# Performance work log

Measured on AMD Instinct MI355X. Metric: run time of the kernel, lower is better.

The kernel has to match this reference:

```python
import jax, jax.numpy as jnp
import numpy as np

N_NODES = 100000
N_EDGES = 1600000
N_GRAPHS = 1024
HID = 128
NODE_DIM = 7
EDGE_DIM = 3
LAYERS = 4
LN_EPS = 1e-5


def setup_inputs() -> dict:
    key = jax.random.key(0)
    ks = jax.random.split(key, 24)
    s = lambda i, shape, scale=0.05: (jax.random.normal(ks[i], shape, dtype=jnp.float32) * scale)
    x = jax.random.normal(ks[0], (N_NODES, NODE_DIM), dtype=jnp.float32)
    edge_index = jax.random.randint(ks[1], (2, N_EDGES), 0, N_NODES, dtype=jnp.int32)
    edge_attr = jax.random.normal(ks[2], (N_EDGES, EDGE_DIM), dtype=jnp.float32)
    batch = jnp.sort(jax.random.randint(ks[3], (N_NODES,), 0, N_GRAPHS, dtype=jnp.int32))
    return {
        'x': x, 'edge_index': edge_index, 'edge_attr': edge_attr, 'batch': batch,
        'inW': s(4, (NODE_DIM, HID)), 'inb': s(5, (HID,)),
        'edgeW': s(6, (LAYERS, EDGE_DIM, HID)), 'edgeb': s(7, (LAYERS, HID)),
        'w1': s(8, (LAYERS, HID, HID)), 'b1': s(9, (LAYERS, HID)),
        'w2': s(10, (LAYERS, HID, HID)), 'b2': s(11, (LAYERS, HID)),
        'gamma': jnp.ones((LAYERS, HID), dtype=jnp.float32),
        'beta': jnp.zeros((LAYERS, HID), dtype=jnp.float32),
        'fcW1': s(12, (HID, HID)), 'fcb1': s(13, (HID,)),
        'fcW2': s(14, (HID, HID // 2)), 'fcb2': s(15, (HID // 2,)),
        'fcW3': s(16, (HID // 2, 1)), 'fcb3': s(17, (1,)),
    }


def _layernorm(x, gamma, beta):
    mu = jnp.mean(x, axis=-1, keepdims=True)
    var = jnp.mean(jnp.square(x - mu), axis=-1, keepdims=True)
    return (x - mu) * jax.lax.rsqrt(var + LN_EPS) * gamma + beta


def reference(x, edge_index, edge_attr, batch, inW, inb, edgeW, edgeb,
              w1, b1, w2, b2, gamma, beta, fcW1, fcb1, fcW2, fcb2, fcW3, fcb3):
    src, dst = edge_index[0], edge_index[1]
    h = x @ inW + inb  # [N, HID]
    for l in range(LAYERS):
        e = edge_attr @ edgeW[l] + edgeb[l]              # [E, HID]
        msg = jax.nn.relu(h[src] + e)                    # gather + relu
        agg = jax.ops.segment_sum(msg, dst, num_segments=N_NODES)  # scatter-add
        g = agg + h                                      # (1+eps)*x_r with eps=0
        g = jax.nn.relu(g @ w1[l] + b1[l]) @ w2[l] + b2[l]  # GINE MLP
        h = _layernorm(h + jax.nn.relu(g), gamma[l], beta[l])  # residual + LN
    # global mean pool over graphs
    sums = jax.ops.segment_sum(h, batch, num_segments=N_GRAPHS)
    cnt = jax.ops.segment_sum(jnp.ones((h.shape[0],), h.dtype), batch, num_segments=N_GRAPHS)
    pooled = sums / jnp.maximum(cnt, 1.0)[:, None]
    # head (dropout is identity in eval)
    o = jax.nn.relu(pooled @ fcW1 + fcb1)
    o = jax.nn.relu(o @ fcW2 + fcb2)
    return o @ fcW3 + fcb3  # [N_GRAPHS, 1]
```

## Files before the change

kernel.cpp:

```cpp
#include <hip/hip_runtime.h>

#define N_NODES 100000
#define N_EDGES 1600000
#define N_GRAPHS 1024
#define HID 128
#define LAYERS 4
#define LN_EPS 1e-5f
#define GTS 136
#define NB_PROJ 50000
#define NB_WCONV 512
#define NBUCK 1563
#define BCAP 2048
#define NSTREAM 8
#define CURPAD 32
#define EPB 4096
#define NB_BS 391


typedef __attribute__((ext_vector_type(8))) short bf16x8;
typedef __attribute__((ext_vector_type(4))) float f32x4;

__device__ __forceinline__ unsigned short f2bf(float x) {
    unsigned v = __float_as_uint(x);
    return (unsigned short)((v + 0x7fffu + ((v >> 16) & 1u)) >> 16);
}
__device__ __forceinline__ float bfval(unsigned short u) {
    return __uint_as_float((unsigned)u << 16);
}

__global__ __launch_bounds__(256) void k_prep(
    const float* __restrict__ x, const float* __restrict__ inW,
    const float* __restrict__ inb, float* __restrict__ h,
    unsigned short* __restrict__ hb,
    const float* __restrict__ w1, const float* __restrict__ w2,
    unsigned short* __restrict__ wf_hi, unsigned short* __restrict__ wf_lo) {
    if (blockIdx.x < NB_PROJ) {
        int idx = blockIdx.x * 256 + threadIdx.x;
        int n = idx >> 7, c = idx & 127;
        const float* xr = x + n * 7;
        float s = inb[c];
#pragma unroll
        for (int k = 0; k < 7; ++k) s += xr[k] * inW[k * HID + c];
        h[idx] = s;
        hb[idx] = f2bf(s);
    } else {
        int idx = (blockIdx.x - NB_PROJ) * 256 + threadIdx.x;
        int wid = idx >> 14;
        int layer = wid >> 1, which = wid & 1;
        int within = idx & 16383;
        int nt = within >> 11;
        int ks = (within >> 9) & 3;
        int ln = (within >> 3) & 63;
        int j = within & 7;
        const float* W = (which ? w2 : w1) + layer * HID * HID;
        int k = ks * 32 + (ln >> 4) * 8 + j;
        int n = nt * 16 + (ln & 15);
        float v = W[k * HID + n];
        unsigned short hi = f2bf(v);
        wf_hi[idx] = hi;
        wf_lo[idx] = f2bf(v - bfval(hi));
    }
}

__global__ __launch_bounds__(256) void k_hist(
    const int* __restrict__ ei, int* __restrict__ cnt2) {
    __shared__ int hcnt[NBUCK];
    const int t = threadIdx.x;
    for (int i = t; i < NBUCK; i += 256) hcnt[i] = 0;
    __syncthreads();
    const int e0 = blockIdx.x * EPB;
    const int eend = (e0 + EPB < N_EDGES) ? e0 + EPB : N_EDGES;
#pragma unroll
    for (int k = 0; k < 16; ++k) {
        const int e = e0 + k * 256 + t;
        if (e < eend) atomicAdd(&hcnt[ei[N_EDGES + e] >> 6], 1);
    }
    __syncthreads();
    const int sgrp = blockIdx.x & 7;
    for (int i = t; i < NBUCK; i += 256) {
        const int c = hcnt[i];
        if (c) atomicAdd(&cnt2[((i << 3) + sgrp) << 5], c);
    }
}

__global__ __launch_bounds__(1024) void k_segscan(
    const int* __restrict__ cnt2, int* __restrict__ pcur,
    int* __restrict__ bucket_base, int* __restrict__ row_ptr) {
    __shared__ int lsum[1024];
    const int t = threadIdx.x;
    const int b0 = 2 * t, b1 = 2 * t + 1;
    int u0 = 0, u1 = 0;
    if (b0 < NBUCK) {
#pragma unroll
        for (int s = 0; s < NSTREAM; ++s) u0 += cnt2[((b0 << 3) + s) << 5];
    }
    if (b1 < NBUCK) {
#pragma unroll
        for (int s = 0; s < NSTREAM; ++s) u1 += cnt2[((b1 << 3) + s) << 5];
    }
    const int v = u0 + u1;
    lsum[t] = v;
    __syncthreads();
    for (int off = 1; off < 1024; off <<= 1) {
        const int u = (t >= off) ? lsum[t - off] : 0;
        __syncthreads();
        lsum[t] += u;
        __syncthreads();
    }
    const int excl = lsum[t] - v;
    if (b0 < NBUCK) {
        bucket_base[b0] = excl;
        int run = excl;
#pragma unroll
        for (int s = 0; s < NSTREAM; ++s) {
            const int c = ((b0 << 3) + s) << 5;
            pcur[c] = run;
            run += cnt2[c];
        }
    }
    if (b1 < NBUCK) {
        const int base1 = excl + u0;
        bucket_base[b1] = base1;
        int run = base1;
#pragma unroll
        for (int s = 0; s < NSTREAM; ++s) {
            const int c = ((b1 << 3) + s) << 5;
            pcur[c] = run;
            run += cnt2[c];
        }
    }
    if (t == 0) {
        bucket_base[NBUCK] = N_EDGES;
        row_ptr[N_NODES] = N_EDGES;
    }
}

__global__ __launch_bounds__(256) void k_binscat(
    const int* __restrict__ ei, const float* __restrict__ ea,
    int* __restrict__ pcur, int4* __restrict__ erec) {
    __shared__ int hcnt[NBUCK];
    const int t = threadIdx.x;
    for (int i = t; i < NBUCK; i += 256) hcnt[i] = 0;
    __syncthreads();
    const int e0 = blockIdx.x * EPB;
    const int eend = (e0 + EPB < N_EDGES) ? e0 + EPB : N_EDGES;
#pragma unroll
    for (int k = 0; k < 16; ++k) {
        const int e = e0 + k * 256 + t;
        if (e < eend) atomicAdd(&hcnt[ei[N_EDGES + e] >> 6], 1);
    }
    __syncthreads();
    const int sgrp = blockIdx.x & 7;
    for (int i = t; i < NBUCK; i += 256) {
        const int c = hcnt[i];
        hcnt[i] = c ? atomicAdd(&pcur[((i << 3) + sgrp) << 5], c) : 0;
    }
    __syncthreads();
#pragma unroll
    for (int k = 0; k < 16; ++k) {
        const int e = e0 + k * 256 + t;
        if (e < eend) {
            const int src = ei[e];
            const int dst = ei[N_EDGES + e];
            const float a0 = ea[e * 3 + 0];
            const float a1 = ea[e * 3 + 1];
            const float a2 = ea[e * 3 + 2];
            const int pos = atomicAdd(&hcnt[dst >> 6], 1);
            int4 r;
            r.x = src | ((dst & 63) << 20);
            r.y = __float_as_int(a0);
            r.z = __float_as_int(a1);
            r.w = __float_as_int(a2);
            erec[pos] = r;
        }
    }
}

__global__ __launch_bounds__(256) void k_bucketsort(
    const int4* __restrict__ erec, const int* __restrict__ bucket_base,
    int* __restrict__ row_ptr, int* __restrict__ esrc,
    float* __restrict__ eattr) {
    __shared__ int rhist[64];
    __shared__ int lcur[64];
    __shared__ int4 stage[BCAP];
    const int b = blockIdx.x;
    const int nb0 = b << 6;
    const int nrows = (nb0 + 64 <= N_NODES) ? 64 : (N_NODES - nb0);
    const int base = bucket_base[b];
    const int end = bucket_base[b + 1];
    const int cnt = end - base;
    const int t = threadIdx.x;
    if (t < 64) rhist[t] = 0;
    __syncthreads();
    for (int i = t; i < cnt; i += 256)
        atomicAdd(&rhist[(erec[base + i].x >> 20) & 63], 1);
    __syncthreads();
    if (t < 64) {
        const int v = rhist[t];
        int incl = v;
#pragma unroll
        for (int off = 1; off < 64; off <<= 1) {
            const int u = __shfl_up(incl, off);
            if (t >= off) incl += u;
        }
        const int excl = incl - v;
        lcur[t] = excl;
        if (t < nrows) row_ptr[nb0 + t] = base + excl;
    }
    __syncthreads();
    if (cnt <= BCAP) {
        for (int i = t; i < cnt; i += 256) {
            const int4 r = erec[base + i];
            stage[atomicAdd(&lcur[(r.x >> 20) & 63], 1)] = r;
        }
        __syncthreads();
        for (int i = t; i < cnt; i += 256)
            esrc[base + i] = stage[i].x & 0xFFFFF;
        float* ef = eattr + (size_t)base * 3;
        const float* sf = (const float*)stage;
        const int m = cnt * 3;
        for (int i = t; i < m; i += 256)
            ef[i] = sf[(i / 3) * 4 + 1 + (i % 3)];
    } else {
        for (int i = t; i < cnt; i += 256) {
            const int4 r = erec[base + i];
            const int pos = base + atomicAdd(&lcur[(r.x >> 20) & 63], 1);
            esrc[pos] = r.x & 0xFFFFF;
            eattr[(size_t)pos * 3 + 0] = __int_as_float(r.y);
            eattr[(size_t)pos * 3 + 1] = __int_as_float(r.z);
            eattr[(size_t)pos * 3 + 2] = __int_as_float(r.w);
        }
    }
}

#define FLUSHSTEP {                                                            \
    if (rcur == 0)      { a0x = ax; a0y = ay; rnext = rp2; }                   \
    else if (rcur == 1) { a1x = ax; a1y = ay; rnext = rp3; }                   \
    else                { a2x = ax; a2y = ay; rnext = 0x7fffffff; }            \
    ax = 0.f; ay = 0.f; ++rcur; }

#define EL(JJ)                                                                 \
    const int s##JJ = __builtin_amdgcn_readlane(cS, j + JJ);                   \
    const unsigned gq##JJ = *(const unsigned*)(hbin + (long)s##JJ * HID + c2);

#define EC(JJ) {                                                               \
    const int gi = t + j + (JJ);                                               \
    while (gi >= rnext) FLUSHSTEP                                              \
    const float ax_ = __uint_as_float(__builtin_amdgcn_readlane(__float_as_int(cA0), j + JJ)); \
    const float ay_ = __uint_as_float(__builtin_amdgcn_readlane(__float_as_int(cA1), j + JJ)); \
    const float az_ = __uint_as_float(__builtin_amdgcn_readlane(__float_as_int(cA2), j + JJ)); \
    const float gx = __uint_as_float(gq##JJ << 16) + ebv.x;                    \
    const float gy = __uint_as_float(gq##JJ & 0xffff0000u) + ebv.y;            \
    const float mx = fmaxf(fmaf(az_, ew2.x, fmaf(ay_, ew1.x, fmaf(ax_, ew0.x, gx))), 0.f); \
    const float my = fmaxf(fmaf(az_, ew2.y, fmaf(ay_, ew1.y, fmaf(ax_, ew0.y, gy))), 0.f); \
    ax += mx; ay += my; }

#define ROW_OUT(R, AX, AY) {                                                   \
    const float2 hv = *(const float2*)(h + (long)(nb + (R)) * HID + c2);       \
    const float gx = hv.x + (AX), gy = hv.y + (AY);                            \
    const unsigned short hx = f2bf(gx), hy = f2bf(gy);                         \
    const unsigned short lx = f2bf(gx - bfval(hx)), ly = f2bf(gy - bfval(hy)); \
    *(unsigned*)&gt_hi[(r0 + (R)) * GTS + c2] = (unsigned)hx | ((unsigned)hy << 16); \
    *(unsigned*)&gt_lo[(r0 + (R)) * GTS + c2] = (unsigned)lx | ((unsigned)ly << 16); }

#define T1_OUT(CC, NT) {                                                       \
    const float4 bv = *(const float4*)(b1 + (NT) * 16 + q4);                   \
    const float v0 = fmaxf(CC[0] + bv.x, 0.f);                                 \
    const float v1 = fmaxf(CC[1] + bv.y, 0.f);                                 \
    const float v2 = fmaxf(CC[2] + bv.z, 0.f);                                 \
    const float v3 = fmaxf(CC[3] + bv.w, 0.f);                                 \
    const unsigned short h0_ = f2bf(v0), h1_ = f2bf(v1), h2_ = f2bf(v2), h3_ = f2bf(v3); \
    const unsigned short l0_ = f2bf(v0 - bfval(h0_)), l1_ = f2bf(v1 - bfval(h1_)); \
    const unsigned short l2_ = f2bf(v2 - bfval(h2_)), l3_ = f2bf(v3 - bfval(h3_)); \
    *(uint2*)&t1_hi[ln15 * GTS + (NT) * 16 + q4] =                             \
        make_uint2((unsigned)h0_ | ((unsigned)h1_ << 16), (unsigned)h2_ | ((unsigned)h3_ << 16)); \
    *(uint2*)&t1_lo[ln15 * GTS + (NT) * 16 + q4] =                             \
        make_uint2((unsigned)l0_ | ((unsigned)l1_ << 16), (unsigned)l2_ | ((unsigned)l3_ << 16)); }

__global__ __launch_bounds__(256, 8) void k_node_update(
    const int* __restrict__ esrc, const float* __restrict__ eattr,
    const int* __restrict__ row_ptr,
    const float* __restrict__ eW, const float* __restrict__ eb,
    float* __restrict__ h, const unsigned short* __restrict__ hbin,
    unsigned short* __restrict__ hbout,
    const unsigned short* __restrict__ w1f_hi, const unsigned short* __restrict__ w1f_lo,
    const unsigned short* __restrict__ w2f_hi, const unsigned short* __restrict__ w2f_lo,
    const float* __restrict__ b1, const float* __restrict__ b2,
    const float* __restrict__ gamma, const float* __restrict__ beta) {
    __shared__ __align__(16) unsigned char smem[17408];
    float* stats = (float*)smem;
    unsigned short* gt_hi = (unsigned short*)(smem + 0);
    unsigned short* gt_lo = (unsigned short*)(smem + 4352);
    unsigned short* t1_hi = (unsigned short*)(smem + 8704);
    unsigned short* t1_lo = (unsigned short*)(smem + 13056);

    const int wave = threadIdx.x >> 6;
    const int lane = threadIdx.x & 63;
    const int n0 = blockIdx.x * 16;
    const int r0 = wave * 4;
    const int c2 = lane * 2;

    {
        const float2 ew0 = *(const float2*)(eW + 0 * HID + c2);
        const float2 ew1 = *(const float2*)(eW + 1 * HID + c2);
        const float2 ew2 = *(const float2*)(eW + 2 * HID + c2);
        const float2 ebv = *(const float2*)(eb + c2);
        const int nb = n0 + r0;
        const int rp0 = __builtin_amdgcn_readfirstlane(row_ptr[nb + 0]);
        const int rp1 = __builtin_amdgcn_readfirstlane(row_ptr[nb + 1]);
        const int rp2 = __builtin_amdgcn_readfirstlane(row_ptr[nb + 2]);
        const int rp3 = __builtin_amdgcn_readfirstlane(row_ptr[nb + 3]);
        const int rp4 = __builtin_amdgcn_readfirstlane(row_ptr[nb + 4]);

        float a0x = 0.f, a0y = 0.f, a1x = 0.f, a1y = 0.f;
        float a2x = 0.f, a2y = 0.f, a3x = 0.f, a3y = 0.f;
        float ax = 0.f, ay = 0.f;
        int rcur = 0;
        int rnext = rp1;

        int cS, nS;
        float cA0, cA1, cA2, nA0, nA1, nA2;
        if (rp0 + lane < rp4) {
            cS = esrc[rp0 + lane];
            cA0 = eattr[(size_t)(rp0 + lane) * 3 + 0];
            cA1 = eattr[(size_t)(rp0 + lane) * 3 + 1];
            cA2 = eattr[(size_t)(rp0 + lane) * 3 + 2];
        }
        for (int t = rp0; t < rp4; t += 64) {
            const int cnt = (rp4 - t < 64) ? (rp4 - t) : 64;
            if (t + 64 + lane < rp4) {
                nS = esrc[t + 64 + lane];
                nA0 = eattr[(size_t)(t + 64 + lane) * 3 + 0];
                nA1 = eattr[(size_t)(t + 64 + lane) * 3 + 1];
                nA2 = eattr[(size_t)(t + 64 + lane) * 3 + 2];
            }
            int j = 0;
            for (; j + 16 <= cnt; j += 16) {
                EL(0) EL(1) EL(2) EL(3) EL(4) EL(5) EL(6) EL(7)
                EL(8) EL(9) EL(10) EL(11) EL(12) EL(13) EL(14) EL(15)
                EC(0) EC(1) EC(2) EC(3) EC(4) EC(5) EC(6) EC(7)
                EC(8) EC(9) EC(10) EC(11) EC(12) EC(13) EC(14) EC(15)
            }
            for (; j + 4 <= cnt; j += 4) {
                EL(0) EL(1) EL(2) EL(3)
                EC(0) EC(1) EC(2) EC(3)
            }
            for (; j < cnt; ++j) {
                EL(0)
                EC(0)
            }
            cS = nS; cA0 = nA0; cA1 = nA1; cA2 = nA2;
        }
        if (rcur == 0)      { a0x = ax; a0y = ay; }
        else if (rcur == 1) { a1x = ax; a1y = ay; }
        else if (rcur == 2) { a2x = ax; a2y = ay; }
        else                { a3x = ax; a3y = ay; }
        ROW_OUT(0, a0x, a0y)
        ROW_OUT(1, a1x, a1y)
        ROW_OUT(2, a2x, a2y)
        ROW_OUT(3, a3x, a3y)
    }
    __syncthreads();

    const int ln15 = lane & 15;
    const int q8 = (lane >> 4) * 8;
    const int q4 = (lane >> 4) * 4;
    const int nt0 = wave * 2, nt1 = nt0 + 1;

    {
        f32x4 c0 = {0.f, 0.f, 0.f, 0.f};
        f32x4 c1 = {0.f, 0.f, 0.f, 0.f};
#pragma unroll
        for (int ks = 0; ks < 4; ++ks) {
            const bf16x8 bh = *(const bf16x8*)&gt_hi[ln15 * GTS + ks * 32 + q8];
            const bf16x8 bl = *(const bf16x8*)&gt_lo[ln15 * GTS + ks * 32 + q8];
            const bf16x8 a0h = *(const bf16x8*)(w1f_hi + (((nt0 * 4 + ks) * 64 + lane) << 3));
            const bf16x8 a0l = *(const bf16x8*)(w1f_lo + (((nt0 * 4 + ks) * 64 + lane) << 3));
            const bf16x8 a1h = *(const bf16x8*)(w1f_hi + (((nt1 * 4 + ks) * 64 + lane) << 3));
            const bf16x8 a1l = *(const bf16x8*)(w1f_lo + (((nt1 * 4 + ks) * 64 + lane) << 3));
            c0 = __builtin_amdgcn_mfma_f32_16x16x32_bf16(a0h, bh, c0, 0, 0, 0);
            c0 = __builtin_amdgcn_mfma_f32_16x16x32_bf16(a0h, bl, c0, 0, 0, 0);
            c0 = __builtin_amdgcn_mfma_f32_16x16x32_bf16(a0l, bh, c0, 0, 0, 0);
            c1 = __builtin_amdgcn_mfma_f32_16x16x32_bf16(a1h, bh, c1, 0, 0, 0);
            c1 = __builtin_amdgcn_mfma_f32_16x16x32_bf16(a1h, bl, c1, 0, 0, 0);
            c1 = __builtin_amdgcn_mfma_f32_16x16x32_bf16(a1l, bh, c1, 0, 0, 0);
        }
        T1_OUT(c0, nt0)
        T1_OUT(c1, nt1)
    }
    __syncthreads();

    {
        f32x4 c0 = {0.f, 0.f, 0.f, 0.f};
        f32x4 c1 = {0.f, 0.f, 0.f, 0.f};
#pragma unroll
        for (int ks = 0; ks < 4; ++ks) {
            const bf16x8 bh = *(const bf16x8*)&t1_hi[ln15 * GTS + ks * 32 + q8];
            const bf16x8 bl = *(const bf16x8*)&t1_lo[ln15 * GTS + ks * 32 + q8];
            const bf16x8 a0h = *(const bf16x8*)(w2f_hi + (((nt0 * 4 + ks) * 64 + lane) << 3));
            const bf16x8 a0l = *(const bf16x8*)(w2f_lo + (((nt0 * 4 + ks) * 64 + lane) << 3));
            const bf16x8 a1h = *(const bf16x8*)(w2f_hi + (((nt1 * 4 + ks) * 64 + lane) << 3));
            const bf16x8 a1l = *(const bf16x8*)(w2f_lo + (((nt1 * 4 + ks) * 64 + lane) << 3));
            c0 = __builtin_amdgcn_mfma_f32_16x16x32_bf16(a0h, bh, c0, 0, 0, 0);
            c0 = __builtin_amdgcn_mfma_f32_16x16x32_bf16(a0h, bl, c0, 0, 0, 0);
            c0 = __builtin_amdgcn_mfma_f32_16x16x32_bf16(a0l, bh, c0, 0, 0, 0);
            c1 = __builtin_amdgcn_mfma_f32_16x16x32_bf16(a1h, bh, c1, 0, 0, 0);
            c1 = __builtin_amdgcn_mfma_f32_16x16x32_bf16(a1h, bl, c1, 0, 0, 0);
            c1 = __builtin_amdgcn_mfma_f32_16x16x32_bf16(a1l, bh, c1, 0, 0, 0);
        }
        const int row = n0 + ln15;
        const float4 b20 = *(const float4*)(b2 + nt0 * 16 + q4);
        const float4 b21 = *(const float4*)(b2 + nt1 * 16 + q4);
        const float4 hv0 = *(const float4*)(h + (long)row * HID + nt0 * 16 + q4);
        const float4 hv1 = *(const float4*)(h + (long)row * HID + nt1 * 16 + q4);
        float4 u0, u1;
        u0.x = hv0.x + fmaxf(c0[0] + b20.x, 0.f);
        u0.y = hv0.y + fmaxf(c0[1] + b20.y, 0.f);
        u0.z = hv0.z + fmaxf(c0[2] + b20.z, 0.f);
        u0.w = hv0.w + fmaxf(c0[3] + b20.w, 0.f);
        u1.x = hv1.x + fmaxf(c1[0] + b21.x, 0.f);
        u1.y = hv1.y + fmaxf(c1[1] + b21.y, 0.f);
        u1.z = hv1.z + fmaxf(c1[2] + b21.z, 0.f);
        u1.w = hv1.w + fmaxf(c1[3] + b21.w, 0.f);
        float s = u0.x + u0.y + u0.z + u0.w + u1.x + u1.y + u1.z + u1.w;
        float s2 = u0.x * u0.x + u0.y * u0.y + u0.z * u0.z + u0.w * u0.w +
                   u1.x * u1.x + u1.y * u1.y + u1.z * u1.z + u1.w * u1.w;
        s += __shfl_xor(s, 16); s2 += __shfl_xor(s2, 16);
        s += __shfl_xor(s, 32); s2 += __shfl_xor(s2, 32);
        if (lane < 16) {
            stats[wave * 32 + lane * 2 + 0] = s;
            stats[wave * 32 + lane * 2 + 1] = s2;
        }
        __syncthreads();
        const float S  = stats[0 * 32 + ln15 * 2] + stats[1 * 32 + ln15 * 2] +
                         stats[2 * 32 + ln15 * 2] + stats[3 * 32 + ln15 * 2];
        const float S2 = stats[0 * 32 + ln15 * 2 + 1] + stats[1 * 32 + ln15 * 2 + 1] +
                         stats[2 * 32 + ln15 * 2 + 1] + stats[3 * 32 + ln15 * 2 + 1];
        const float mu = S * (1.f / HID);
        const float var = S2 * (1.f / HID) - mu * mu;
        const float inv = rsqrtf(var + LN_EPS);
        const float4 gm0 = *(const float4*)(gamma + nt0 * 16 + q4);
        const float4 gm1 = *(const float4*)(gamma + nt1 * 16 + q4);
        const float4 bt0 = *(const float4*)(beta + nt0 * 16 + q4);
        const float4 bt1 = *(const float4*)(beta + nt1 * 16 + q4);
        float4 o0, o1;
        o0.x = (u0.x - mu) * inv * gm0.x + bt0.x;
        o0.y = (u0.y - mu) * inv * gm0.y + bt0.y;
        o0.z = (u0.z - mu) * inv * gm0.z + bt0.z;
        o0.w = (u0.w - mu) * inv * gm0.w + bt0.w;
        o1.x = (u1.x - mu) * inv * gm1.x + bt1.x;
        o1.y = (u1.y - mu) * inv * gm1.y + bt1.y;
        o1.z = (u1.z - mu) * inv * gm1.z + bt1.z;
        o1.w = (u1.w - mu) * inv * gm1.w + bt1.w;
        *(float4*)(h + (long)row * HID + nt0 * 16 + q4) = o0;
        *(float4*)(h + (long)row * HID + nt1 * 16 + q4) = o1;
        *(uint2*)(hbout + (long)row * HID + nt0 * 16 + q4) =
            make_uint2((unsigned)f2bf(o0.x) | ((unsigned)f2bf(o0.y) << 16),
                       (unsigned)f2bf(o0.z) | ((unsigned)f2bf(o0.w) << 16));
        *(uint2*)(hbout + (long)row * HID + nt1 * 16 + q4) =
            make_uint2((unsigned)f2bf(o1.x) | ((unsigned)f2bf(o1.y) << 16),
                       (unsigned)f2bf(o1.z) | ((unsigned)f2bf(o1.w) << 16));
    }
}

__global__ __launch_bounds__(128) void k_pool(
    const float* __restrict__ h, const int* __restrict__ batch,
    float* __restrict__ sums, float* __restrict__ cnt) {
    const int c = threadIdx.x;
    const int n0 = blockIdx.x * 64;
    if (n0 >= N_NODES) return;
    const int nend = min(n0 + 64, N_NODES);
    int cur = batch[n0];
    float acc = 0.f;
    int runlen = 0;
    for (int n = n0; n < nend; ++n) {
        const int b = batch[n];
        if (b != cur) {
            atomicAdd(&sums[(long)cur * HID + c], acc);
            if (c == 0) atomicAdd(&cnt[cur], (float)runlen);
            acc = 0.f;
            runlen = 0;
            cur = b;
        }
        acc += h[(long)n * HID + c];
        ++runlen;
    }
    atomicAdd(&sums[(long)cur * HID + c], acc);
    if (c == 0) atomicAdd(&cnt[cur], (float)runlen);
}

__global__ __launch_bounds__(128) void k_head(
    const float* __restrict__ sums, const float* __restrict__ cnt,
    const float* __restrict__ fcW1, const float* __restrict__ fcb1,
    const float* __restrict__ fcW2, const float* __restrict__ fcb2,
    const float* __restrict__ fcW3, const float* __restrict__ fcb3,
    float* __restrict__ out) {
    __shared__ float p[HID];
    __shared__ float o1[HID];
    __shared__ float o2[64];
    const int g = blockIdx.x, t = threadIdx.x;
    const float c = fmaxf(cnt[g], 1.0f);
    p[t] = sums[g * HID + t] / c;
    __syncthreads();
    float s = fcb1[t];
    for (int k = 0; k < HID; ++k) s += p[k] * fcW1[k * HID + t];
    o1[t] = fmaxf(s, 0.f);
    __syncthreads();
    if (t < 64) {
        float s2 = fcb2[t];
        for (int k = 0; k < HID; ++k) s2 += o1[k] * fcW2[k * 64 + t];
        o2[t] = fmaxf(s2, 0.f);
    }
    __syncthreads();
    if (t < 64) {
        float v = o2[t] * fcW3[t];
#pragma unroll
        for (int off = 32; off > 0; off >>= 1) v += __shfl_down(v, off);
        if (t == 0) out[g] = v + fcb3[0];
    }
}

extern "C" void kernel_launch(void* const* d_in, const int* in_sizes, int n_in,
                              void* d_out, int out_size, void* d_ws, size_t ws_size,
                              hipStream_t stream) {
    const float* x    = (const float*)d_in[0];
    const int*   ei   = (const int*)d_in[1];
    const float* ea   = (const float*)d_in[2];
    const int*   batch= (const int*)d_in[3];
    const float* inW  = (const float*)d_in[4];
    const float* inb  = (const float*)d_in[5];
    const float* edgeW= (const float*)d_in[6];
    const float* edgeb= (const float*)d_in[7];
    const float* w1   = (const float*)d_in[8];
    const float* b1   = (const float*)d_in[9];
    const float* w2   = (const float*)d_in[10];
    const float* b2   = (const float*)d_in[11];
    const float* gamma= (const float*)d_in[12];
    const float* beta = (const float*)d_in[13];
    const float* fcW1 = (const float*)d_in[14];
    const float* fcb1 = (const float*)d_in[15];
    const float* fcW2 = (const float*)d_in[16];
    const float* fcb2 = (const float*)d_in[17];
    const float* fcW3 = (const float*)d_in[18];
    const float* fcb3 = (const float*)d_in[19];
    float* out = (float*)d_out;

    float* eattr = (float*)d_ws;
    float* h     = eattr + (size_t)N_EDGES * 3;
    unsigned short* hb0 = (unsigned short*)(h + (size_t)N_NODES * HID);
    unsigned short* hb1 = hb0 + (size_t)N_NODES * HID;
    unsigned short* wf_hi = hb1 + (size_t)N_NODES * HID;
    unsigned short* wf_lo = wf_hi + LAYERS * 2 * 16384;
    int*    esrc    = (int*)(wf_lo + LAYERS * 2 * 16384);
    int*    row_ptr = esrc + N_EDGES;
    int*    pcur    = (int*)(((size_t)(row_ptr + (N_NODES + 1)) + 127) & ~(size_t)127);
    int*    bucket_base = pcur + NBUCK * NSTREAM * CURPAD;
    int*    cnt2    = (int*)(((size_t)(bucket_base + NBUCK + 1) + 127) & ~(size_t)127);
    float*  sums    = (float*)(cnt2 + NBUCK * NSTREAM * CURPAD);
    float*  cnt     = sums + (size_t)N_GRAPHS * HID;
    const size_t zbytes = (size_t)NBUCK * NSTREAM * CURPAD * sizeof(int) +
                          ((size_t)N_GRAPHS * HID + N_GRAPHS) * sizeof(float);
    int4*   erec    = (int4*)hb1;

    hipMemsetAsync(cnt2, 0, zbytes, stream);

    k_prep<<<NB_PROJ + NB_WCONV, 256, 0, stream>>>(x, inW, inb, h, hb0,
                                                   w1, w2, wf_hi, wf_lo);

    k_hist<<<NB_BS, 256, 0, stream>>>(ei, cnt2);
    k_segscan<<<1, 1024, 0, stream>>>(cnt2, pcur, bucket_base, row_ptr);
    k_binscat<<<NB_BS, 256, 0, stream>>>(ei, ea, pcur, erec);
    k_bucketsort<<<NBUCK, 256, 0, stream>>>(erec, bucket_base, row_ptr,
                                            esrc, eattr);

    unsigned short* hbin = hb0;
    unsigned short* hbout = hb1;
    for (int l = 0; l < LAYERS; ++l) {
        k_node_update<<<N_NODES / 16, 256, 0, stream>>>(
            esrc, eattr, row_ptr, edgeW + l * 3 * HID, edgeb + l * HID,
            h, hbin, hbout,
            wf_hi + (l * 2 + 0) * 16384, wf_lo + (l * 2 + 0) * 16384,
            wf_hi + (l * 2 + 1) * 16384, wf_lo + (l * 2 + 1) * 16384,
            b1 + l * HID, b2 + l * HID, gamma + l * HID, beta + l * HID);
        unsigned short* tmp = hbin; hbin = hbout; hbout = tmp;
    }

    k_pool<<<(N_NODES + 63) / 64, 128, 0, stream>>>(h, batch, sums, cnt);
    k_head<<<N_GRAPHS, 128, 0, stream>>>(sums, cnt, fcW1, fcb1, fcW2, fcb2,
                                         fcW3, fcb3, out);
}
```

Baseline: 695.8 us.

## Pack edge src and attrs into int4 records and use packed FMA in aggregation

Bucket sort now writes one int4 per edge (source index plus three attributes) in place of separate esrc and eattr arrays, so each edge is fetched with a single 16-byte load in the node update. Edge attributes are staged in per-wave shared memory, already duplicated into pairs, instead of being broadcast with three readlanes per edge. The message compute and accumulation use v_pk_fma_f32/v_pk_add_f32 on float pairs. This cuts scalar readlane and VALU work in the gather loop, at the cost of extra LDS traffic, slightly more bytes per edge, and a dependence on smem space beyond the prior layout.

```diff
diff --git a/kernel.cpp b/kernel.cpp
--- a/kernel.cpp
+++ b/kernel.cpp
@@ -19,6 +19,7 @@
 
 typedef __attribute__((ext_vector_type(8))) short bf16x8;
 typedef __attribute__((ext_vector_type(4))) float f32x4;
+typedef __attribute__((ext_vector_type(2))) float f32x2;
 
 __device__ __forceinline__ unsigned short f2bf(float x) {
     unsigned v = __float_as_uint(x);
@@ -26,6 +27,16 @@
 }
 __device__ __forceinline__ float bfval(unsigned short u) {
     return __uint_as_float((unsigned)u << 16);
+}
+__device__ __forceinline__ f32x2 pk_fma(f32x2 a, f32x2 b, f32x2 c) {
+    f32x2 d;
+    asm("v_pk_fma_f32 %0, %1, %2, %3" : "=v"(d) : "v"(a), "v"(b), "v"(c));
+    return d;
+}
+__device__ __forceinline__ f32x2 pk_add(f32x2 a, f32x2 b) {
+    f32x2 d;
+    asm("v_pk_add_f32 %0, %1, %2" : "=v"(d) : "v"(a), "v"(b));
+    return d;
 }
 
 __global__ __launch_bounds__(256) void k_prep(
@@ -178,8 +189,7 @@
 
 __global__ __launch_bounds__(256) void k_bucketsort(
     const int4* __restrict__ erec, const int* __restrict__ bucket_base,
-    int* __restrict__ row_ptr, int* __restrict__ esrc,
-    float* __restrict__ eattr) {
+    int* __restrict__ row_ptr, int4* __restrict__ edata) {
     __shared__ int rhist[64];
     __shared__ int lcur[64];
     __shared__ int4 stage[BCAP];
@@ -214,30 +224,27 @@
             stage[atomicAdd(&lcur[(r.x >> 20) & 63], 1)] = r;
         }
         __syncthreads();
-        for (int i = t; i < cnt; i += 256)
-            esrc[base + i] = stage[i].x & 0xFFFFF;
-        float* ef = eattr + (size_t)base * 3;
-        const float* sf = (const float*)stage;
-        const int m = cnt * 3;
-        for (int i = t; i < m; i += 256)
-            ef[i] = sf[(i / 3) * 4 + 1 + (i % 3)];
+        for (int i = t; i < cnt; i += 256) {
+            int4 r = stage[i];
+            r.x &= 0xFFFFF;
+            edata[base + i] = r;
+        }
     } else {
         for (int i = t; i < cnt; i += 256) {
             const int4 r = erec[base + i];
             const int pos = base + atomicAdd(&lcur[(r.x >> 20) & 63], 1);
-            esrc[pos] = r.x & 0xFFFFF;
-            eattr[(size_t)pos * 3 + 0] = __int_as_float(r.y);
-            eattr[(size_t)pos * 3 + 1] = __int_as_float(r.z);
-            eattr[(size_t)pos * 3 + 2] = __int_as_float(r.w);
+            int4 o = r;
+            o.x = r.x & 0xFFFFF;
+            edata[pos] = o;
         }
     }
 }
 
 #define FLUSHSTEP {                                                            \
-    if (rcur == 0)      { a0x = ax; a0y = ay; rnext = rp2; }                   \
-    else if (rcur == 1) { a1x = ax; a1y = ay; rnext = rp3; }                   \
-    else                { a2x = ax; a2y = ay; rnext = 0x7fffffff; }            \
-    ax = 0.f; ay = 0.f; ++rcur; }
+    if (rcur == 0)      { a0v = acc2; rnext = rp2; }                           \
+    else if (rcur == 1) { a1v = acc2; rnext = rp3; }                           \
+    else                { a2v = acc2; rnext = 0x7fffffff; }                    \
+    acc2[0] = 0.f; acc2[1] = 0.f; ++rcur; }
 
 #define EL(JJ)                                                                 \
     const int s##JJ = __builtin_amdgcn_readlane(cS, j + JJ);                   \
@@ -246,18 +253,20 @@
 #define EC(JJ) {                                                               \
     const int gi = t + j + (JJ);                                               \
     while (gi >= rnext) FLUSHSTEP                                              \
-    const float ax_ = __uint_as_float(__builtin_amdgcn_readlane(__float_as_int(cA0), j + JJ)); \
-    const float ay_ = __uint_as_float(__builtin_amdgcn_readlane(__float_as_int(cA1), j + JJ)); \
-    const float az_ = __uint_as_float(__builtin_amdgcn_readlane(__float_as_int(cA2), j + JJ)); \
-    const float gx = __uint_as_float(gq##JJ << 16) + ebv.x;                    \
-    const float gy = __uint_as_float(gq##JJ & 0xffff0000u) + ebv.y;            \
-    const float mx = fmaxf(fmaf(az_, ew2.x, fmaf(ay_, ew1.x, fmaf(ax_, ew0.x, gx))), 0.f); \
-    const float my = fmaxf(fmaf(az_, ew2.y, fmaf(ay_, ew1.y, fmaf(ax_, ew0.y, gy))), 0.f); \
-    ax += mx; ay += my; }
-
-#define ROW_OUT(R, AX, AY) {                                                   \
+    const f32x4 qq = attAB[j + (JJ)];                                          \
+    const f32x2 pC = attC[j + (JJ)];                                           \
+    f32x2 pA; pA[0] = qq[0]; pA[1] = qq[1];                                    \
+    f32x2 pB; pB[0] = qq[2]; pB[1] = qq[3];                                    \
+    f32x2 g2; g2[0] = __uint_as_float(gq##JJ << 16);                           \
+    g2[1] = __uint_as_float(gq##JJ & 0xffff0000u);                             \
+    const f32x2 m2 = pk_fma(pC, ew2v, pk_fma(pB, ew1v, pk_fma(pA, ew0v,        \
+                            pk_add(g2, ebv2))));                               \
+    f32x2 r2; r2[0] = fmaxf(m2[0], 0.f); r2[1] = fmaxf(m2[1], 0.f);            \
+    acc2 = pk_add(acc2, r2); }
+
+#define ROW_OUT(R, AV) {                                                       \
     const float2 hv = *(const float2*)(h + (long)(nb + (R)) * HID + c2);       \
-    const float gx = hv.x + (AX), gy = hv.y + (AY);                            \
+    const float gx = hv.x + (AV)[0], gy = hv.y + (AV)[1];                      \
     const unsigned short hx = f2bf(gx), hy = f2bf(gy);                         \
     const unsigned short lx = f2bf(gx - bfval(hx)), ly = f2bf(gy - bfval(hy)); \
     *(unsigned*)&gt_hi[(r0 + (R)) * GTS + c2] = (unsigned)hx | ((unsigned)hy << 16); \
@@ -278,8 +287,7 @@
         make_uint2((unsigned)l0_ | ((unsigned)l1_ << 16), (unsigned)l2_ | ((unsigned)l3_ << 16)); }
 
 __global__ __launch_bounds__(256, 8) void k_node_update(
-    const int* __restrict__ esrc, const float* __restrict__ eattr,
-    const int* __restrict__ row_ptr,
+    const int4* __restrict__ edata, const int* __restrict__ row_ptr,
     const float* __restrict__ eW, const float* __restrict__ eb,
     float* __restrict__ h, const unsigned short* __restrict__ hbin,
     unsigned short* __restrict__ hbout,
@@ -301,10 +309,12 @@
     const int c2 = lane * 2;
 
     {
-        const float2 ew0 = *(const float2*)(eW + 0 * HID + c2);
-        const float2 ew1 = *(const float2*)(eW + 1 * HID + c2);
-        const float2 ew2 = *(const float2*)(eW + 2 * HID + c2);
-        const float2 ebv = *(const float2*)(eb + c2);
+        f32x4* attAB = (f32x4*)(smem + 8704 + wave * 1536);
+        f32x2* attC  = (f32x2*)(smem + 8704 + wave * 1536 + 1024);
+        const f32x2 ew0v = *(const f32x2*)(eW + 0 * HID + c2);
+        const f32x2 ew1v = *(const f32x2*)(eW + 1 * HID + c2);
+        const f32x2 ew2v = *(const f32x2*)(eW + 2 * HID + c2);
+        const f32x2 ebv2 = *(const f32x2*)(eb + c2);
         const int nb = n0 + r0;
         const int rp0 = __builtin_amdgcn_readfirstlane(row_ptr[nb + 0]);
         const int rp1 = __builtin_amdgcn_readfirstlane(row_ptr[nb + 1]);
@@ -312,28 +322,27 @@
         const int rp3 = __builtin_amdgcn_readfirstlane(row_ptr[nb + 3]);
         const int rp4 = __builtin_amdgcn_readfirstlane(row_ptr[nb + 4]);
 
-        float a0x = 0.f, a0y = 0.f, a1x = 0.f, a1y = 0.f;
-        float a2x = 0.f, a2y = 0.f, a3x = 0.f, a3y = 0.f;
-        float ax = 0.f, ay = 0.f;
+        f32x2 a0v = {0.f, 0.f}, a1v = {0.f, 0.f};
+        f32x2 a2v = {0.f, 0.f}, a3v = {0.f, 0.f};
+        f32x2 acc2 = {0.f, 0.f};
         int rcur = 0;
         int rnext = rp1;
 
-        int cS, nS;
-        float cA0, cA1, cA2, nA0, nA1, nA2;
-        if (rp0 + lane < rp4) {
-            cS = esrc[rp0 + lane];
-            cA0 = eattr[(size_t)(rp0 + lane) * 3 + 0];
-            cA1 = eattr[(size_t)(rp0 + lane) * 3 + 1];
-            cA2 = eattr[(size_t)(rp0 + lane) * 3 + 2];
-        }
+        int4 cE = {0, 0, 0, 0}, nE = {0, 0, 0, 0};
+        if (rp0 + lane < rp4) cE = edata[rp0 + lane];
         for (int t = rp0; t < rp4; t += 64) {
             const int cnt = (rp4 - t < 64) ? (rp4 - t) : 64;
-            if (t + 64 + lane < rp4) {
-                nS = esrc[t + 64 + lane];
-                nA0 = eattr[(size_t)(t + 64 + lane) * 3 + 0];
-                nA1 = eattr[(size_t)(t + 64 + lane) * 3 + 1];
-                nA2 = eattr[(size_t)(t + 64 + lane) * 3 + 2];
-            }
+            f32x4 dAB;
+            dAB[0] = __int_as_float(cE.y); dAB[1] = dAB[0];
+            dAB[2] = __int_as_float(cE.z); dAB[3] = dAB[2];
+            f32x2 dC;
+            dC[0] = __int_as_float(cE.w); dC[1] = dC[0];
+            attAB[lane] = dAB;
+            attC[lane] = dC;
+            const int cS = cE.x;
+            __builtin_amdgcn_wave_barrier();
+            if (t + 64 + lane < rp4)
+                nE = edata[t + 64 + lane];
             int j = 0;
             for (; j + 16 <= cnt; j += 16) {
                 EL(0) EL(1) EL(2) EL(3) EL(4) EL(5) EL(6) EL(7)
@@ -349,16 +358,17 @@
                 EL(0)
                 EC(0)
             }
-            cS = nS; cA0 = nA0; cA1 = nA1; cA2 = nA2;
-        }
-        if (rcur == 0)      { a0x = ax; a0y = ay; }
-        else if (rcur == 1) { a1x = ax; a1y = ay; }
-        else if (rcur == 2) { a2x = ax; a2y = ay; }
-        else                { a3x = ax; a3y = ay; }
-        ROW_OUT(0, a0x, a0y)
-        ROW_OUT(1, a1x, a1y)
-        ROW_OUT(2, a2x, a2y)
-        ROW_OUT(3, a3x, a3y)
+            __builtin_amdgcn_wave_barrier();
+            cE = nE;
+        }
+        if (rcur == 0)      a0v = acc2;
+        else if (rcur == 1) a1v = acc2;
+        else if (rcur == 2) a2v = acc2;
+        else                a3v = acc2;
+        ROW_OUT(0, a0v)
+        ROW_OUT(1, a1v)
+        ROW_OUT(2, a2v)
+        ROW_OUT(3, a3v)
     }
     __syncthreads();
 
@@ -545,14 +555,13 @@
     const float* fcb3 = (const float*)d_in[19];
     float* out = (float*)d_out;
 
-    float* eattr = (float*)d_ws;
-    float* h     = eattr + (size_t)N_EDGES * 3;
+    int4*  edata = (int4*)d_ws;
+    float* h     = (float*)(edata + (size_t)N_EDGES);
     unsigned short* hb0 = (unsigned short*)(h + (size_t)N_NODES * HID);
     unsigned short* hb1 = hb0 + (size_t)N_NODES * HID;
     unsigned short* wf_hi = hb1 + (size_t)N_NODES * HID;
     unsigned short* wf_lo = wf_hi + LAYERS * 2 * 16384;
-    int*    esrc    = (int*)(wf_lo + LAYERS * 2 * 16384);
-    int*    row_ptr = esrc + N_EDGES;
+    int*    row_ptr = (int*)(wf_lo + LAYERS * 2 * 16384);
     int*    pcur    = (int*)(((size_t)(row_ptr + (N_NODES + 1)) + 127) & ~(size_t)127);
     int*    bucket_base = pcur + NBUCK * NSTREAM * CURPAD;
     int*    cnt2    = (int*)(((size_t)(bucket_base + NBUCK + 1) + 127) & ~(size_t)127);
@@ -570,14 +579,13 @@
     k_hist<<<NB_BS, 256, 0, stream>>>(ei, cnt2);
     k_segscan<<<1, 1024, 0, stream>>>(cnt2, pcur, bucket_base, row_ptr);
     k_binscat<<<NB_BS, 256, 0, stream>>>(ei, ea, pcur, erec);
-    k_bucketsort<<<NBUCK, 256, 0, stream>>>(erec, bucket_base, row_ptr,
-                                            esrc, eattr);
+    k_bucketsort<<<NBUCK, 256, 0, stream>>>(erec, bucket_base, row_ptr, edata);
 
     unsigned short* hbin = hb0;
     unsigned short* hbout = hb1;
     for (int l = 0; l < LAYERS; ++l) {
         k_node_update<<<N_NODES / 16, 256, 0, stream>>>(
-            esrc, eattr, row_ptr, edgeW + l * 3 * HID, edgeb + l * HID,
+            edata, row_ptr, edgeW + l * 3 * HID, edgeb + l * HID,
             h, hbin, hbout,
             wf_hi + (l * 2 + 0) * 16384, wf_lo + (l * 2 + 0) * 16384,
             wf_hi + (l * 2 + 1) * 16384, wf_lo + (l * 2 + 1) * 16384,
```

Result: no change. 704.2 us (+1.2%).
